# Performance work log

Hardware: AMD Instinct MI355X
Metric: run time of the kernel (lower is better)

The kernel has to match this reference:

```python
import jax, jax.numpy as jnp
import numpy as np

N_NODES = 100000
N_EDGES = 3200000
IN_DIM = 128
HIDDEN = 128
NUM_GRAPHS = 512


def setup_inputs() -> dict:
    key = jax.random.key(0)
    ks = jax.random.split(key, 12)
    x = jax.random.normal(ks[0], (N_NODES, IN_DIM), dtype=jnp.float32)
    edge_index = jax.random.randint(ks[1], (2, N_EDGES), 0, N_NODES, dtype=jnp.int64)
    edge_attr = jax.random.normal(ks[2], (N_EDGES, 4), dtype=jnp.float32)
    batch = jnp.sort(jax.random.randint(ks[3], (N_NODES,), 0, NUM_GRAPHS, dtype=jnp.int64))

    def glorot(k, fin, fout):
        s = np.float32(np.sqrt(2.0 / (fin + fout)))
        return jax.random.normal(k, (fin, fout), dtype=jnp.float32) * s

    W0 = glorot(ks[4], IN_DIM, HIDDEN); b0 = jnp.zeros((HIDDEN,), jnp.float32)
    W1 = glorot(ks[5], HIDDEN, HIDDEN); b1 = jnp.zeros((HIDDEN,), jnp.float32)
    W2 = glorot(ks[6], HIDDEN, HIDDEN); b2 = jnp.zeros((HIDDEN,), jnp.float32)
    Wm0 = glorot(ks[7], HIDDEN, HIDDEN); bm0 = jnp.zeros((HIDDEN,), jnp.float32)
    Wm1 = glorot(ks[8], HIDDEN, 1); bm1 = jnp.zeros((1,), jnp.float32)
    return {"x": x, "edge_index": edge_index, "edge_attr": edge_attr, "batch": batch,
            "W0": W0, "b0": b0, "W1": W1, "b1": b1, "W2": W2, "b2": b2,
            "Wm0": Wm0, "bm0": bm0, "Wm1": Wm1, "bm1": bm1}


def reference(x, edge_index, edge_attr, batch, W0, b0, W1, b1, W2, b2, Wm0, bm0, Wm1, bm1):
    # edge_attr is accepted but unused, matching the original GCNConv call.
    N = x.shape[0]
    row = edge_index[0]
    col = edge_index[1]
    # PyG gcn_norm: add self-loops, deg from target index (col), symmetric norm.
    loop = jnp.arange(N, dtype=row.dtype)
    row = jnp.concatenate([row, loop])
    col = jnp.concatenate([col, loop])
    deg = jax.ops.segment_sum(jnp.ones(row.shape, jnp.float32), col, num_segments=N)
    dis = jnp.where(deg > 0, jax.lax.rsqrt(jnp.maximum(deg, 1.0)), 0.0)
    norm = dis[row] * dis[col]  # [E+N]

    def gcn_conv(h, W, b):
        h = h @ W                                  # [N, H] transform first (PyG order)
        msg = h[row] * norm[:, None]               # gather + scale, [E+N, H]
        agg = jax.ops.segment_sum(msg, col, num_segments=N)  # scatter-add
        return agg + b

    h = jax.nn.relu(gcn_conv(x, W0, b0))  # dropout inactive in eval mode
    h = jax.nn.relu(gcn_conv(h, W1, b1))
    h = jax.nn.relu(gcn_conv(h, W2, b2))

    # global_mean_pool: segment mean over graph ids
    sums = jax.ops.segment_sum(h, batch, num_segments=NUM_GRAPHS)
    cnt = jax.ops.segment_sum(jnp.ones((N,), jnp.float32), batch, num_segments=NUM_GRAPHS)
    g = sums / jnp.maximum(cnt, 1.0)[:, None]      # [G, H]

    g = jax.nn.relu(g @ Wm0 + bm0)
    return g @ Wm1 + bm1                           # [G, 1]
```

## Files before the change

kernel.cpp:

```cpp
#include <hip/hip_runtime.h>
#include <hip/hip_fp16.h>


#define HID 128
#define NGR 512
#define NB_SHIFT 9
#define NB_W 512
#define EPB 4096

typedef __attribute__((ext_vector_type(8))) _Float16 half8;
typedef __attribute__((ext_vector_type(4))) float floatx4;


__global__ __launch_bounds__(256) void k_hist(const int* __restrict__ col,
                                              int* __restrict__ ghist, int E, int nb) {
    __shared__ int h[256];
    h[threadIdx.x] = 0;
    __syncthreads();
    for (int e = blockIdx.x * 256 + threadIdx.x; e < E; e += gridDim.x * 256)
        atomicAdd(&h[col[e] >> NB_SHIFT], 1);
    __syncthreads();
    int t = threadIdx.x;
    if (t < nb && h[t]) atomicAdd(&ghist[t], h[t]);
}

__global__ __launch_bounds__(256) void k_bscan(const int* __restrict__ ghist,
                                               int* __restrict__ bbase,
                                               int* __restrict__ rowptr,
                                               int N, int E, int nb) {
    __shared__ int wsum[4];
    int t = threadIdx.x, lane = t & 63, wid = t >> 6;
    int v = (t < nb) ? ghist[t] : 0;
    int sc = v;
    #pragma unroll
    for (int off = 1; off < 64; off <<= 1) {
        int u = __shfl_up(sc, off);
        if (lane >= off) sc += u;
    }
    if (lane == 63) wsum[wid] = sc;
    __syncthreads();
    int offs = 0;
    for (int w = 0; w < wid; w++) offs += wsum[w];
    int excl = offs + sc - v;
    if (t <= nb) bbase[t] = excl;
    if (t == 0) rowptr[N] = E;
}

__global__ __launch_bounds__(256) void k_scatter(const int* __restrict__ row,
                                                 const int* __restrict__ col,
                                                 const int* __restrict__ bbase,
                                                 int* __restrict__ bcur,
                                                 unsigned* __restrict__ sorted, int E) {
    __shared__ int hist[256];
    __shared__ int cur[256];
    int t = threadIdx.x;
    hist[t] = 0;
    __syncthreads();
    int base = blockIdx.x * EPB;
    #pragma unroll
    for (int i = 0; i < EPB / 256; i++) {
        int e = base + i * 256 + t;
        if (e < E) atomicAdd(&hist[col[e] >> NB_SHIFT], 1);
    }
    __syncthreads();
    if (hist[t] > 0) cur[t] = atomicAdd(&bcur[t], hist[t]);
    __syncthreads();
    #pragma unroll
    for (int i = 0; i < EPB / 256; i++) {
        int e = base + i * 256 + t;
        if (e < E) {
            int d = col[e], b = d >> NB_SHIFT;
            int p = atomicAdd(&cur[b], 1);
            sorted[bbase[b] + p] = ((unsigned)row[e] << NB_SHIFT) | (unsigned)(d & (NB_W - 1));
        }
    }
}

__global__ __launch_bounds__(256) void k_build(const unsigned* __restrict__ sorted,
                                               const int* __restrict__ bbase,
                                               int* __restrict__ csr_src,
                                               int* __restrict__ rowptr,
                                               float* __restrict__ dis, int N) {
    __shared__ int cnt[NB_W];
    __shared__ int excl[NB_W];
    __shared__ int wsum[4];
    int b = blockIdx.x, t = threadIdx.x;
    cnt[t] = 0; cnt[t + 256] = 0;
    __syncthreads();
    int s0 = bbase[b], s1 = bbase[b + 1];
    for (int p = s0 + t; p < s1; p += 256)
        atomicAdd(&cnt[sorted[p] & (NB_W - 1)], 1);
    __syncthreads();
    int c0 = cnt[2 * t], c1 = cnt[2 * t + 1];
    int v = c0 + c1, lane = t & 63, wid = t >> 6;
    int sc = v;
    #pragma unroll
    for (int off = 1; off < 64; off <<= 1) {
        int u = __shfl_up(sc, off);
        if (lane >= off) sc += u;
    }
    if (lane == 63) wsum[wid] = sc;
    __syncthreads();
    int offs = 0;
    for (int w = 0; w < wid; w++) offs += wsum[w];
    int e0 = offs + sc - v;
    excl[2 * t] = e0;
    excl[2 * t + 1] = e0 + c0;
    int dbase = b << NB_SHIFT;
    int d0 = dbase + 2 * t, d1 = d0 + 1;
    if (d0 < N) { rowptr[d0] = s0 + e0;      dis[d0] = rsqrtf((float)(c0 + 1)); }
    if (d1 < N) { rowptr[d1] = s0 + e0 + c0; dis[d1] = rsqrtf((float)(c1 + 1)); }
    __syncthreads();
    for (int p = s0 + t; p < s1; p += 256) {
        unsigned sd = sorted[p];
        int q = atomicAdd(&excl[sd & (NB_W - 1)], 1);
        csr_src[s0 + q] = (int)(sd >> NB_SHIFT);
    }
}


__global__ __launch_bounds__(256) void k_wprep(const float* __restrict__ W0,
                                               const float* __restrict__ W1,
                                               const float* __restrict__ W2,
                                               _Float16* __restrict__ Wt) {
    int l = blockIdx.x >> 4;
    int chunk = blockIdx.x & 15;
    const float* W = (l == 0) ? W0 : (l == 1) ? W1 : W2;
    _Float16* D = Wt + (size_t)l * HID * HID;
    int t = threadIdx.x;
    int k  = chunk * 8 + (t >> 5);
    int n0 = (t & 31) * 4;
    float4 v = *(const float4*)(W + (size_t)k * HID + n0);
    D[(size_t)(n0 + 0) * HID + k] = (_Float16)v.x;
    D[(size_t)(n0 + 1) * HID + k] = (_Float16)v.y;
    D[(size_t)(n0 + 2) * HID + k] = (_Float16)v.z;
    D[(size_t)(n0 + 3) * HID + k] = (_Float16)v.w;
}


__device__ __forceinline__ half8 load_afrag(const float* A, int arow, int k0, int N) {
    const float* p = A + (size_t)arow * HID + k0;
    float4 v0 = *(const float4*)p;
    float4 v1 = *(const float4*)(p + 4);
    half8 h;
    h[0] = (_Float16)v0.x; h[1] = (_Float16)v0.y;
    h[2] = (_Float16)v0.z; h[3] = (_Float16)v0.w;
    h[4] = (_Float16)v1.x; h[5] = (_Float16)v1.y;
    h[6] = (_Float16)v1.z; h[7] = (_Float16)v1.w;
    return h;
}
__device__ __forceinline__ half8 load_afrag(const _Float16* A, int arow, int k0, int N) {
    return *(const half8*)(A + ((size_t)(k0 >> 6) * N + arow) * 64 + (k0 & 63));
}

template <typename AT>
__global__ __launch_bounds__(256, 2) void k_gemm(const AT* __restrict__ A,
                                                 const _Float16* __restrict__ Wt,
                                                 const float* __restrict__ dis,
                                                 __half* __restrict__ C, int N) {
    const int lane = threadIdx.x & 63;
    const int quad = lane >> 4;
    const int mc   = lane & 15;
    const int gw   = (blockIdx.x * 256 + threadIdx.x) >> 6;
    const int nw   = (gridDim.x * 256) >> 6;
    const int nstrips = (N + 15) >> 4;

    half8 b[8][4];
    #pragma unroll
    for (int j = 0; j < 8; j++)
        #pragma unroll
        for (int s = 0; s < 4; s++)
            b[j][s] = *(const half8*)(Wt + (size_t)(j * 16 + mc) * HID + s * 32 + quad * 8);

    int strip = gw;
    if (strip >= nstrips) return;

    half8 a[4];
    {
        int arow = strip * 16 + mc; if (arow >= N) arow = N - 1;
        #pragma unroll
        for (int s = 0; s < 4; s++) a[s] = load_afrag(A, arow, s * 32 + quad * 8, N);
    }

    for (; strip < nstrips; strip += nw) {
        const int row0 = strip * 16;
        const int next = strip + nw;
        half8 an[4];
        if (next < nstrips) {
            int arow = next * 16 + mc; if (arow >= N) arow = N - 1;
            #pragma unroll
            for (int s = 0; s < 4; s++) an[s] = load_afrag(A, arow, s * 32 + quad * 8, N);
        }
        floatx4 acc[8];
        #pragma unroll
        for (int j = 0; j < 8; j++) acc[j] = (floatx4){0.f, 0.f, 0.f, 0.f};
        #pragma unroll
        for (int s = 0; s < 4; s++)
            #pragma unroll
            for (int j = 0; j < 8; j++)
                acc[j] = __builtin_amdgcn_mfma_f32_16x16x32_f16(a[s], b[j][s], acc[j], 0, 0, 0);
        #pragma unroll
        for (int r = 0; r < 4; r++) {
            int gr = row0 + quad * 4 + r;
            if (gr < N) {
                float ds = dis[gr];
                #pragma unroll
                for (int j = 0; j < 8; j++)
                    C[((size_t)(j >> 2) * N + gr) * 64 + (j & 3) * 16 + mc] =
                        __float2half(ds * acc[j][r]);
            }
        }
        #pragma unroll
        for (int s = 0; s < 4; s++) a[s] = an[s];
    }
}


__device__ __forceinline__ void add8(float* acc, float4 r) {
    __half2* h = (__half2*)&r;
    #pragma unroll
    for (int k = 0; k < 4; k++) {
        float2 v = __half22float2(h[k]);
        acc[2 * k]     += v.x;
        acc[2 * k + 1] += v.y;
    }
}

__global__ __launch_bounds__(256) void k_agg(const __half* __restrict__ T,
                                             const float* __restrict__ dis,
                                             const int* __restrict__ rowptr,
                                             const int* __restrict__ csr_src,
                                             const float* __restrict__ bias,
                                             __half* __restrict__ out, int N) {
    const int pass = blockIdx.y;
    const int g    = threadIdx.x >> 5;
    const int l    = threadIdx.x & 31;
    const int p    = l >> 3;
    const int h    = l & 7;
    const int n = blockIdx.x * 8 + g;
    if (n >= N) return;

    const float4* T4 = (const float4*)(T + (size_t)pass * N * 64);

    float acc[8] = {};

    int e  = rowptr[n];
    int e1 = rowptr[n + 1];
    for (; e + 16 <= e1; e += 16) {
        int s0 = csr_src[e + p];
        int s1 = csr_src[e + 4 + p];
        int s2 = csr_src[e + 8 + p];
        int s3 = csr_src[e + 12 + p];
        float4 r0 = T4[(size_t)s0 * 8 + h];
        float4 r1 = T4[(size_t)s1 * 8 + h];
        float4 r2 = T4[(size_t)s2 * 8 + h];
        float4 r3 = T4[(size_t)s3 * 8 + h];
        add8(acc, r0); add8(acc, r1); add8(acc, r2); add8(acc, r3);
    }
    for (; e + 4 <= e1; e += 4) {
        int s = csr_src[e + p];
        add8(acc, T4[(size_t)s * 8 + h]);
    }
    if (e + p < e1) {
        int s = csr_src[e + p];
        add8(acc, T4[(size_t)s * 8 + h]);
    }
    if (p == 0) add8(acc, T4[(size_t)n * 8 + h]);

    #pragma unroll
    for (int k = 0; k < 8; k++) {
        acc[k] += __shfl_xor(acc[k], 8, 64);
        acc[k] += __shfl_xor(acc[k], 16, 64);
    }

    if (p == 0) {
        float dn = dis[n];
        half8 o;
        #pragma unroll
        for (int k = 0; k < 8; k++) {
            float v = fmaf(dn, acc[k], bias[pass * 64 + h * 8 + k]);
            o[k] = (_Float16)fmaxf(v, 0.f);
        }
        *(half8*)((_Float16*)out + ((size_t)pass * N + n) * 64 + h * 8) = o;
    }
}


__device__ __forceinline__ int lbound(const int* __restrict__ batch, int N, int g) {
    int lo = 0, hi = N;
    while (lo < hi) {
        int mid = (lo + hi) >> 1;
        if (batch[mid] < g) lo = mid + 1; else hi = mid;
    }
    return lo;
}

__global__ __launch_bounds__(128) void k_pool(const __half* __restrict__ h,
                                              const int* __restrict__ batch,
                                              float* __restrict__ g, int N) {
    int gr = blockIdx.x;
    int f  = threadIdx.x;
    int s = lbound(batch, N, gr), e = lbound(batch, N, gr + 1);
    const __half* hs = h + (size_t)(f >> 6) * N * 64;
    int c = f & 63;
    float acc = 0.f;
    for (int r = s; r < e; r++) acc += __half2float(hs[(size_t)r * 64 + c]);
    g[gr * HID + f] = acc / fmaxf((float)(e - s), 1.f);
}


__global__ __launch_bounds__(128) void k_mlp(const float* __restrict__ g,
                                             const float* __restrict__ Wm0,
                                             const float* __restrict__ bm0,
                                             const float* __restrict__ Wm1,
                                             const float* __restrict__ bm1,
                                             float* __restrict__ out) {
    __shared__ float gl[HID];
    __shared__ float red[HID];
    int gr = blockIdx.x, j = threadIdx.x;
    gl[j] = g[gr * HID + j];
    __syncthreads();
    float acc = bm0[j];
    for (int k = 0; k < HID; k++) acc = fmaf(gl[k], Wm0[k * HID + j], acc);
    acc = fmaxf(acc, 0.f);
    red[j] = acc * Wm1[j];
    __syncthreads();
    for (int off = 64; off > 0; off >>= 1) {
        if (j < off) red[j] += red[j + off];
        __syncthreads();
    }
    if (j == 0) out[gr] = red[0] + bm1[0];
}


extern "C" void kernel_launch(void* const* d_in, const int* in_sizes, int n_in,
                              void* d_out, int out_size, void* d_ws, size_t ws_size,
                              hipStream_t stream) {
    const float* x     = (const float*)d_in[0];
    const int*   ei    = (const int*)d_in[1];
    const int*   batch = (const int*)d_in[3];
    const float* W0 = (const float*)d_in[4],  *b0 = (const float*)d_in[5];
    const float* W1 = (const float*)d_in[6],  *b1 = (const float*)d_in[7];
    const float* W2 = (const float*)d_in[8],  *b2 = (const float*)d_in[9];
    const float* Wm0 = (const float*)d_in[10], *bm0 = (const float*)d_in[11];
    const float* Wm1 = (const float*)d_in[12], *bm1 = (const float*)d_in[13];

    const int N = in_sizes[0] / HID;
    const int E = in_sizes[1] / 2;
    const int nb = (N + NB_W - 1) >> NB_SHIFT;
    const int* row  = ei;
    const int* colI = ei + E;

    char* w = (char*)d_ws;
    auto carve = [&](size_t bytes) {
        void* p = (void*)w;
        w += (bytes + 255) & ~(size_t)255;
        return p;
    };
    int*      ibuf    = (int*)     carve(512 * 4);
    int*      bbase   = (int*)     carve(257 * 4);
    float*    dis     = (float*)   carve((size_t)N * 4);
    int*      rowptr  = (int*)     carve((size_t)(N + 1) * 4);
    unsigned* sorted  = (unsigned*)carve((size_t)E * 4);
    int*      csr_src = (int*)     carve((size_t)E * 4);
    _Float16* wth     = (_Float16*)carve((size_t)3 * HID * HID * 2);
    __half*   bufT    = (__half*)  carve((size_t)N * HID * 2);
    __half*   bufA    = (__half*)  carve((size_t)N * HID * 2);
    __half*   bufB    = (__half*)  carve((size_t)N * HID * 2);
    float*    gsum    = (float*)   carve((size_t)NGR * HID * 4);

    int* ghist = ibuf;
    int* bcur  = ibuf + 256;

    hipMemsetAsync(ibuf, 0, 512 * 4, stream);
    k_wprep  <<<48, 256, 0, stream>>>(W0, W1, W2, wth);
    k_hist   <<<512, 256, 0, stream>>>(colI, ghist, E, nb);
    k_bscan  <<<1, 256, 0, stream>>>(ghist, bbase, rowptr, N, E, nb);
    k_scatter<<<(E + EPB - 1) / EPB, 256, 0, stream>>>(row, colI, bbase, bcur, sorted, E);
    k_build  <<<nb, 256, 0, stream>>>(sorted, bbase, csr_src, rowptr, dis, N);

    dim3 gg(512);
    dim3 ga((N + 7) / 8, 2);

    k_gemm<float>    <<<gg, 256, 0, stream>>>(x, wth, dis, bufT, N);
    k_agg            <<<ga, 256, 0, stream>>>(bufT, dis, rowptr, csr_src, b0, bufA, N);
    k_gemm<_Float16> <<<gg, 256, 0, stream>>>((const _Float16*)bufA, wth + HID * HID, dis, bufT, N);
    k_agg            <<<ga, 256, 0, stream>>>(bufT, dis, rowptr, csr_src, b1, bufB, N);
    k_gemm<_Float16> <<<gg, 256, 0, stream>>>((const _Float16*)bufB, wth + 2 * HID * HID, dis, bufT, N);
    k_agg            <<<ga, 256, 0, stream>>>(bufT, dis, rowptr, csr_src, b2, bufA, N);

    k_pool<<<NGR, 128, 0, stream>>>(bufA, batch, gsum, N);
    k_mlp<<<NGR, 128, 0, stream>>>(gsum, Wm0, bm0, Wm1, bm1, (float*)d_out);
}
```

Before: 699.9 us.

## Fuse pooling with MLP head, widen CSR build blocks, unroll aggregation deeper

Merges the global mean pool and the two-layer MLP head into one kernel. The pool now reads half8 vectors across 16 row groups and reduces them in shared memory, which removes the intermediate gsum buffer and one launch. Scatter and CSR-build kernels move to 512-thread blocks, so each thread handles one destination slot in the build scan. The aggregation gather loop gets a 32-edge unrolled stage to keep more loads in flight, at the cost of more registers.

```diff
diff --git a/kernel.cpp b/kernel.cpp
--- a/kernel.cpp
+++ b/kernel.cpp
@@ -46,7 +46,7 @@
     if (t == 0) rowptr[N] = E;
 }
 
-__global__ __launch_bounds__(256) void k_scatter(const int* __restrict__ row,
+__global__ __launch_bounds__(512) void k_scatter(const int* __restrict__ row,
                                                  const int* __restrict__ col,
                                                  const int* __restrict__ bbase,
                                                  int* __restrict__ bcur,
@@ -54,20 +54,20 @@
     __shared__ int hist[256];
     __shared__ int cur[256];
     int t = threadIdx.x;
-    hist[t] = 0;
+    if (t < 256) hist[t] = 0;
     __syncthreads();
     int base = blockIdx.x * EPB;
     #pragma unroll
-    for (int i = 0; i < EPB / 256; i++) {
-        int e = base + i * 256 + t;
+    for (int i = 0; i < EPB / 512; i++) {
+        int e = base + i * 512 + t;
         if (e < E) atomicAdd(&hist[col[e] >> NB_SHIFT], 1);
     }
     __syncthreads();
-    if (hist[t] > 0) cur[t] = atomicAdd(&bcur[t], hist[t]);
-    __syncthreads();
-    #pragma unroll
-    for (int i = 0; i < EPB / 256; i++) {
-        int e = base + i * 256 + t;
+    if (t < 256 && hist[t] > 0) cur[t] = atomicAdd(&bcur[t], hist[t]);
+    __syncthreads();
+    #pragma unroll
+    for (int i = 0; i < EPB / 512; i++) {
+        int e = base + i * 512 + t;
         if (e < E) {
             int d = col[e], b = d >> NB_SHIFT;
             int p = atomicAdd(&cur[b], 1);
@@ -76,23 +76,23 @@
     }
 }
 
-__global__ __launch_bounds__(256) void k_build(const unsigned* __restrict__ sorted,
+__global__ __launch_bounds__(512) void k_build(const unsigned* __restrict__ sorted,
                                                const int* __restrict__ bbase,
                                                int* __restrict__ csr_src,
                                                int* __restrict__ rowptr,
                                                float* __restrict__ dis, int N) {
     __shared__ int cnt[NB_W];
     __shared__ int excl[NB_W];
-    __shared__ int wsum[4];
+    __shared__ int wsum[8];
     int b = blockIdx.x, t = threadIdx.x;
-    cnt[t] = 0; cnt[t + 256] = 0;
+    cnt[t] = 0;
     __syncthreads();
     int s0 = bbase[b], s1 = bbase[b + 1];
-    for (int p = s0 + t; p < s1; p += 256)
+    for (int p = s0 + t; p < s1; p += 512)
         atomicAdd(&cnt[sorted[p] & (NB_W - 1)], 1);
     __syncthreads();
-    int c0 = cnt[2 * t], c1 = cnt[2 * t + 1];
-    int v = c0 + c1, lane = t & 63, wid = t >> 6;
+    int v = cnt[t];
+    int lane = t & 63, wid = t >> 6;
     int sc = v;
     #pragma unroll
     for (int off = 1; off < 64; off <<= 1) {
@@ -104,14 +104,11 @@
     int offs = 0;
     for (int w = 0; w < wid; w++) offs += wsum[w];
     int e0 = offs + sc - v;
-    excl[2 * t] = e0;
-    excl[2 * t + 1] = e0 + c0;
-    int dbase = b << NB_SHIFT;
-    int d0 = dbase + 2 * t, d1 = d0 + 1;
-    if (d0 < N) { rowptr[d0] = s0 + e0;      dis[d0] = rsqrtf((float)(c0 + 1)); }
-    if (d1 < N) { rowptr[d1] = s0 + e0 + c0; dis[d1] = rsqrtf((float)(c1 + 1)); }
-    __syncthreads();
-    for (int p = s0 + t; p < s1; p += 256) {
+    excl[t] = e0;
+    int d = (b << NB_SHIFT) + t;
+    if (d < N) { rowptr[d] = s0 + e0; dis[d] = rsqrtf((float)(v + 1)); }
+    __syncthreads();
+    for (int p = s0 + t; p < s1; p += 512) {
         unsigned sd = sorted[p];
         int q = atomicAdd(&excl[sd & (NB_W - 1)], 1);
         csr_src[s0 + q] = (int)(sd >> NB_SHIFT);
@@ -246,6 +243,26 @@
 
     int e  = rowptr[n];
     int e1 = rowptr[n + 1];
+    for (; e + 32 <= e1; e += 32) {
+        int s0 = csr_src[e + p];
+        int s1 = csr_src[e + 4 + p];
+        int s2 = csr_src[e + 8 + p];
+        int s3 = csr_src[e + 12 + p];
+        int s4 = csr_src[e + 16 + p];
+        int s5 = csr_src[e + 20 + p];
+        int s6 = csr_src[e + 24 + p];
+        int s7 = csr_src[e + 28 + p];
+        float4 r0 = T4[(size_t)s0 * 8 + h];
+        float4 r1 = T4[(size_t)s1 * 8 + h];
+        float4 r2 = T4[(size_t)s2 * 8 + h];
+        float4 r3 = T4[(size_t)s3 * 8 + h];
+        float4 r4 = T4[(size_t)s4 * 8 + h];
+        float4 r5 = T4[(size_t)s5 * 8 + h];
+        float4 r6 = T4[(size_t)s6 * 8 + h];
+        float4 r7 = T4[(size_t)s7 * 8 + h];
+        add8(acc, r0); add8(acc, r1); add8(acc, r2); add8(acc, r3);
+        add8(acc, r4); add8(acc, r5); add8(acc, r6); add8(acc, r7);
+    }
     for (; e + 16 <= e1; e += 16) {
         int s0 = csr_src[e + p];
         int s1 = csr_src[e + 4 + p];
@@ -295,41 +312,56 @@
     return lo;
 }
 
-__global__ __launch_bounds__(128) void k_pool(const __half* __restrict__ h,
-                                              const int* __restrict__ batch,
-                                              float* __restrict__ g, int N) {
-    int gr = blockIdx.x;
-    int f  = threadIdx.x;
-    int s = lbound(batch, N, gr), e = lbound(batch, N, gr + 1);
-    const __half* hs = h + (size_t)(f >> 6) * N * 64;
-    int c = f & 63;
-    float acc = 0.f;
-    for (int r = s; r < e; r++) acc += __half2float(hs[(size_t)r * 64 + c]);
-    g[gr * HID + f] = acc / fmaxf((float)(e - s), 1.f);
-}
-
-
-__global__ __launch_bounds__(128) void k_mlp(const float* __restrict__ g,
-                                             const float* __restrict__ Wm0,
-                                             const float* __restrict__ bm0,
-                                             const float* __restrict__ Wm1,
-                                             const float* __restrict__ bm1,
-                                             float* __restrict__ out) {
-    __shared__ float gl[HID];
-    __shared__ float red[HID];
-    int gr = blockIdx.x, j = threadIdx.x;
-    gl[j] = g[gr * HID + j];
-    __syncthreads();
-    float acc = bm0[j];
-    for (int k = 0; k < HID; k++) acc = fmaf(gl[k], Wm0[k * HID + j], acc);
-    acc = fmaxf(acc, 0.f);
-    red[j] = acc * Wm1[j];
-    __syncthreads();
-    for (int off = 64; off > 0; off >>= 1) {
-        if (j < off) red[j] += red[j + off];
-        __syncthreads();
-    }
-    if (j == 0) out[gr] = red[0] + bm1[0];
+__global__ __launch_bounds__(256) void k_poolmlp(const __half* __restrict__ hbuf,
+                                                 const int* __restrict__ batch,
+                                                 const float* __restrict__ Wm0,
+                                                 const float* __restrict__ bm0,
+                                                 const float* __restrict__ Wm1,
+                                                 const float* __restrict__ bm1,
+                                                 float* __restrict__ out, int N) {
+    __shared__ float red[2048];
+    __shared__ float g[HID];
+    const int gr = blockIdx.x, t = threadIdx.x;
+    const int s = lbound(batch, N, gr), e = lbound(batch, N, gr + 1);
+
+    const int rg = t >> 4, cl = t & 15;
+    const _Float16* base = (const _Float16*)hbuf
+        + (size_t)(cl >> 3) * N * 64 + (size_t)(cl & 7) * 8;
+    float acc[8] = {};
+    for (int r = s + rg; r < e; r += 16) {
+        half8 v = *(const half8*)(base + (size_t)r * 64);
+        #pragma unroll
+        for (int k = 0; k < 8; k++) acc[k] += (float)v[k];
+    }
+    #pragma unroll
+    for (int k = 0; k < 8; k++) red[t * 8 + k] = acc[k];
+    __syncthreads();
+    if (t < 128) {
+        int cl2 = t >> 3, k = t & 7;
+        float sm = 0.f;
+        #pragma unroll
+        for (int rg2 = 0; rg2 < 16; rg2++) sm += red[(rg2 * 16 + cl2) * 8 + k];
+        int feat = (cl2 & 7) * 8 + k + ((cl2 >> 3) ? 64 : 0);
+        g[feat] = sm / fmaxf((float)(e - s), 1.f);
+    }
+    __syncthreads();
+
+    const int j = t & 127, hh = t >> 7;
+    float a = 0.f;
+    for (int k = hh * 64; k < hh * 64 + 64; k++)
+        a = fmaf(g[k], Wm0[(size_t)k * HID + j], a);
+    red[hh * 128 + j] = a;
+    __syncthreads();
+
+    if (t < 128) {
+        float h1 = fmaxf(bm0[j] + red[j] + red[128 + j], 0.f);
+        float z = h1 * Wm1[j];
+        #pragma unroll
+        for (int off = 32; off > 0; off >>= 1) z += __shfl_xor(z, off, 64);
+        if ((t & 63) == 0) red[1024 + (t >> 6)] = z;
+    }
+    __syncthreads();
+    if (t == 0) out[gr] = red[1024] + red[1025] + bm1[0];
 }
 
 
@@ -367,7 +399,6 @@
     __half*   bufT    = (__half*)  carve((size_t)N * HID * 2);
     __half*   bufA    = (__half*)  carve((size_t)N * HID * 2);
     __half*   bufB    = (__half*)  carve((size_t)N * HID * 2);
-    float*    gsum    = (float*)   carve((size_t)NGR * HID * 4);
 
     int* ghist = ibuf;
     int* bcur  = ibuf + 256;
@@ -376,8 +407,8 @@
     k_wprep  <<<48, 256, 0, stream>>>(W0, W1, W2, wth);
     k_hist   <<<512, 256, 0, stream>>>(colI, ghist, E, nb);
     k_bscan  <<<1, 256, 0, stream>>>(ghist, bbase, rowptr, N, E, nb);
-    k_scatter<<<(E + EPB - 1) / EPB, 256, 0, stream>>>(row, colI, bbase, bcur, sorted, E);
-    k_build  <<<nb, 256, 0, stream>>>(sorted, bbase, csr_src, rowptr, dis, N);
+    k_scatter<<<(E + EPB - 1) / EPB, 512, 0, stream>>>(row, colI, bbase, bcur, sorted, E);
+    k_build  <<<nb, 512, 0, stream>>>(sorted, bbase, csr_src, rowptr, dis, N);
 
     dim3 gg(512);
     dim3 ga((N + 7) / 8, 2);
@@ -389,6 +420,5 @@
     k_gemm<_Float16> <<<gg, 256, 0, stream>>>((const _Float16*)bufB, wth + 2 * HID * HID, dis, bufT, N);
     k_agg            <<<ga, 256, 0, stream>>>(bufT, dis, rowptr, csr_src, b2, bufA, N);
 
-    k_pool<<<NGR, 128, 0, stream>>>(bufA, batch, gsum, N);
-    k_mlp<<<NGR, 128, 0, stream>>>(gsum, Wm0, bm0, Wm1, bm1, (float*)d_out);
-}
+    k_poolmlp<<<NGR, 256, 0, stream>>>(bufA, batch, Wm0, bm0, Wm1, bm1, (float*)d_out, N);
+}
```

Measured after the change: 674.9 us. -3.6%, faster.
